# Performance work log

Measured on AMD Instinct MI355X. Metric: run time of the kernel, lower is better.

## Reference

```python
import jax, jax.numpy as jnp
import numpy as np

SEQ_LEN = 4096
INPUT_DIM = 768
DIM = 512
NUM_HEADS = 8
HEAD_DIM = DIM // NUM_HEADS
WINDOW_SIZE = 7
DILATION = 8
HALF_WINDOW = WINDOW_SIZE // 2  # 3
BIDIRECTIONAL = True


def _dilated_mask(seq_len):
    # allowed neighbors of query i: j = i + k*DILATION for k in [-HALF_WINDOW, HALF_WINDOW]
    # (only k<=0 if not bidirectional), clipped to [0, seq_len)
    idx = jnp.arange(seq_len)
    d = idx[None, :] - idx[:, None]  # j - i
    allowed = (d % DILATION == 0) & (jnp.abs(d) <= DILATION * HALF_WINDOW)
    if not BIDIRECTIONAL:
        allowed = allowed & (d <= 0)
    return jnp.where(allowed, 0.0, -jnp.inf).astype(jnp.float32)  # [S, S]


def setup_inputs() -> dict:
    key = jax.random.key(0)
    ks = jax.random.split(key, 6)
    s = 0.02
    return {
        "x": jax.random.normal(ks[0], (SEQ_LEN, INPUT_DIM), dtype=jnp.float32),
        "W_in": jax.random.normal(ks[1], (INPUT_DIM, DIM), dtype=jnp.float32) * s,
        "b_in": jnp.zeros((DIM,), dtype=jnp.float32),
        "W_tse": jax.random.normal(ks[2], (DIM, 3 * DIM), dtype=jnp.float32) * s,
        "W_out": jax.random.normal(ks[3], (DIM, DIM), dtype=jnp.float32) * s,
        "b_out": jnp.zeros((DIM,), dtype=jnp.float32),
    }


def reference(x, W_in, b_in, W_tse, W_out, b_out):
    S = x.shape[0]
    scale = HEAD_DIM ** -0.5
    h = x @ W_in + b_in                                   # [S, DIM]
    tse = (h @ W_tse).reshape(S, 3, NUM_HEADS, HEAD_DIM)   # [S, 3, H, hd]
    q, k, v = tse[:, 0], tse[:, 1], tse[:, 2]              # each [S, H, hd]
    scores = jnp.einsum("shd,thd->hst", q, k) * scale      # [H, S, S]
    scores = scores + _dilated_mask(S)[None, :, :]
    attn = jax.nn.softmax(scores, axis=-1)                 # [H, S, S]
    out = jnp.einsum("hst,thd->shd", attn, v)              # [S, H, hd]
    out = out.reshape(S, DIM)
    return out @ W_out + b_out                              # [S, DIM]
```

## Files before the change

### kernel.cpp

```cpp
#include <hip/hip_runtime.h>
#include <hip/hip_bf16.h>

#define S_LEN 4096
#define IN_DIM 768
#define D_DIM 512
#define N_HEADS 8
#define H_DIM 64
#define TSE_DIM 1536

typedef __attribute__((ext_vector_type(8))) short frag8;
typedef __attribute__((ext_vector_type(4))) float f32x4;

__device__ __forceinline__ unsigned short f2bfbits(float f) {
    unsigned int u = __float_as_uint(f);
    unsigned int r = (u + 0x7FFFu + ((u >> 16) & 1u)) >> 16;
    return (unsigned short)r;
}
__device__ __forceinline__ float bf2f(unsigned short b) {
    return __uint_as_float(((unsigned int)b) << 16);
}

__device__ __forceinline__ void gload_lds16(const void* g, void* l) {
    __builtin_amdgcn_global_load_lds(
        (const __attribute__((address_space(1))) unsigned int*)g,
        (__attribute__((address_space(3))) unsigned int*)l,
        16, 0, 0);
}

__global__ __launch_bounds__(256) void prep_kernel(
        const float4* __restrict__ x4, ushort4* __restrict__ xb4,
        const float* __restrict__ W_in,  unsigned short* __restrict__ WinT,
        const float* __restrict__ W_tse, unsigned short* __restrict__ WtseT,
        const float* __restrict__ W_out, unsigned short* __restrict__ WoutT) {
    __shared__ float tile[32][33];
    int b = blockIdx.x;
    if (b < 3072) {
        int i = b * 256 + threadIdx.x;
        float4 v = x4[i];
        ushort4 o;
        o.x = f2bfbits(v.x); o.y = f2bfbits(v.y);
        o.z = f2bfbits(v.z); o.w = f2bfbits(v.w);
        xb4[i] = o;
        return;
    }
    const float* in; unsigned short* out; int K, N, t;
    if (b < 3456)      { t = b - 3072; in = W_in;  out = WinT;  K = IN_DIM; N = D_DIM;  }
    else if (b < 4224) { t = b - 3456; in = W_tse; out = WtseT; K = D_DIM;  N = TSE_DIM;}
    else               { t = b - 4224; in = W_out; out = WoutT; K = D_DIM;  N = D_DIM;  }
    int ktiles = K / 32;
    int kb = (t % ktiles) * 32, nb = (t / ktiles) * 32;
    int tx = threadIdx.x & 31, ty = threadIdx.x >> 5;
    #pragma unroll
    for (int r = ty; r < 32; r += 8)
        tile[r][tx] = in[(size_t)(kb + r) * N + nb + tx];
    __syncthreads();
    #pragma unroll
    for (int r = ty; r < 32; r += 8)
        out[(size_t)(nb + r) * K + kb + tx] = f2bfbits(tile[tx][r]);
}

template<bool OUT_BF16, bool BIAS>
__global__ __launch_bounds__(256) void gemm_nt(
        const unsigned short* __restrict__ A,
        const unsigned short* __restrict__ Bt,
        const float* __restrict__ bias,
        void* __restrict__ C,
        int M, int N, int K) {
    __shared__ __align__(16) unsigned short As[2][64 * 32];
    __shared__ __align__(16) unsigned short Bs[2][64 * 32];

    const int bm = blockIdx.x * 64;
    const int bn = blockIdx.y * 64;
    const int lane = threadIdx.x & 63;
    const int wave = threadIdx.x >> 6;
    const int wr = wave >> 1;
    const int wc = wave & 1;
    const int fr = lane & 15;
    const int fg = lane >> 4;

    const int srow = lane >> 2;
    const int scol = (lane & 3) * 8;

    const unsigned short* agp = A  + (size_t)(bm + wave * 16 + srow) * K + scol;
    const unsigned short* bgp = Bt + (size_t)(bn + wave * 16 + srow) * K + scol;
    unsigned short* alp0 = &As[0][wave * 512];
    unsigned short* blp0 = &Bs[0][wave * 512];
    unsigned short* alp1 = &As[1][wave * 512];
    unsigned short* blp1 = &Bs[1][wave * 512];

    f32x4 acc[2][2];
    #pragma unroll
    for (int mi = 0; mi < 2; ++mi)
        #pragma unroll
        for (int ni = 0; ni < 2; ++ni)
            acc[mi][ni] = (f32x4)(0.f);

    const int nt = K >> 5;

    gload_lds16(agp, alp0);
    gload_lds16(bgp, blp0);
    __syncthreads();

    int cur = 0;
    for (int kt = 0; kt + 1 < nt; ++kt) {
        const int ko = (kt + 1) << 5;
        gload_lds16(agp + ko, cur ? alp0 : alp1);
        gload_lds16(bgp + ko, cur ? blp0 : blp1);

        frag8 a[2], b[2];
        #pragma unroll
        for (int mi = 0; mi < 2; ++mi)
            a[mi] = *(const frag8*)&As[cur][(wr * 32 + mi * 16 + fr) * 32 + fg * 8];
        #pragma unroll
        for (int ni = 0; ni < 2; ++ni)
            b[ni] = *(const frag8*)&Bs[cur][(wc * 32 + ni * 16 + fr) * 32 + fg * 8];
        #pragma unroll
        for (int mi = 0; mi < 2; ++mi)
            #pragma unroll
            for (int ni = 0; ni < 2; ++ni)
                acc[mi][ni] = __builtin_amdgcn_mfma_f32_16x16x32_bf16(
                        a[mi], b[ni], acc[mi][ni], 0, 0, 0);

        __syncthreads();
        cur ^= 1;
    }

    {
        frag8 a[2], b[2];
        #pragma unroll
        for (int mi = 0; mi < 2; ++mi)
            a[mi] = *(const frag8*)&As[cur][(wr * 32 + mi * 16 + fr) * 32 + fg * 8];
        #pragma unroll
        for (int ni = 0; ni < 2; ++ni)
            b[ni] = *(const frag8*)&Bs[cur][(wc * 32 + ni * 16 + fr) * 32 + fg * 8];
        #pragma unroll
        for (int mi = 0; mi < 2; ++mi)
            #pragma unroll
            for (int ni = 0; ni < 2; ++ni)
                acc[mi][ni] = __builtin_amdgcn_mfma_f32_16x16x32_bf16(
                        a[mi], b[ni], acc[mi][ni], 0, 0, 0);
    }

    #pragma unroll
    for (int mi = 0; mi < 2; ++mi) {
        int grow = bm + wr * 32 + mi * 16 + fg * 4;
        #pragma unroll
        for (int ni = 0; ni < 2; ++ni) {
            int gcol = bn + wc * 32 + ni * 16 + fr;
            float bv = BIAS ? bias[gcol] : 0.f;
            #pragma unroll
            for (int r = 0; r < 4; ++r) {
                float v = acc[mi][ni][r] + bv;
                if (OUT_BF16)
                    ((unsigned short*)C)[(size_t)(grow + r) * N + gcol] = f2bfbits(v);
                else
                    ((float*)C)[(size_t)(grow + r) * N + gcol] = v;
            }
        }
    }
}

__global__ __launch_bounds__(256) void attn_kernel(
        const unsigned short* __restrict__ tse, unsigned short* __restrict__ out) {
    const int s    = blockIdx.x * 4 + (threadIdx.x >> 6);
    const int lane = threadIdx.x & 63;
    const int off  = (lane >> 3) * H_DIM + (lane & 7) * 8;

    float qf[8];
    {
        frag8 q = *(const frag8*)(tse + (size_t)s * TSE_DIM + off);
        #pragma unroll
        for (int i = 0; i < 8; ++i) qf[i] = bf2f((unsigned short)q[i]);
    }

    float sc[7];
    #pragma unroll
    for (int j = 0; j < 7; ++j) {
        int t = s + (j - 3) * 8;
        bool valid = (t >= 0) && (t < S_LEN);
        float p = 0.f;
        if (valid) {
            frag8 k = *(const frag8*)(tse + (size_t)t * TSE_DIM + D_DIM + off);
            #pragma unroll
            for (int i = 0; i < 8; ++i) p += qf[i] * bf2f((unsigned short)k[i]);
        }
        p += __shfl_xor(p, 1, 64);
        p += __shfl_xor(p, 2, 64);
        p += __shfl_xor(p, 4, 64);
        sc[j] = valid ? p * 0.125f : -__builtin_inff();
    }

    float m = sc[0];
    #pragma unroll
    for (int j = 1; j < 7; ++j) m = fmaxf(m, sc[j]);

    float w[7], denom = 0.f;
    #pragma unroll
    for (int j = 0; j < 7; ++j) {
        w[j] = (sc[j] == -__builtin_inff()) ? 0.f : __expf(sc[j] - m);
        denom += w[j];
    }
    const float inv = 1.f / denom;

    float of[8];
    #pragma unroll
    for (int i = 0; i < 8; ++i) of[i] = 0.f;
    #pragma unroll
    for (int j = 0; j < 7; ++j) {
        int t = s + (j - 3) * 8;
        if (t >= 0 && t < S_LEN) {
            frag8 v = *(const frag8*)(tse + (size_t)t * TSE_DIM + 2 * D_DIM + off);
            #pragma unroll
            for (int i = 0; i < 8; ++i) of[i] += w[j] * bf2f((unsigned short)v[i]);
        }
    }

    frag8 o;
    #pragma unroll
    for (int i = 0; i < 8; ++i) o[i] = (short)f2bfbits(of[i] * inv);
    *(frag8*)(out + (size_t)s * D_DIM + off) = o;
}

extern "C" void kernel_launch(void* const* d_in, const int* in_sizes, int n_in,
                              void* d_out, int out_size, void* d_ws, size_t ws_size,
                              hipStream_t stream) {
    (void)in_sizes; (void)n_in; (void)out_size;
    const float* x     = (const float*)d_in[0];
    const float* W_in  = (const float*)d_in[1];
    const float* b_in  = (const float*)d_in[2];
    const float* W_tse = (const float*)d_in[3];
    const float* W_out = (const float*)d_in[4];
    const float* b_out = (const float*)d_in[5];

    char* p = (char*)d_ws;
    unsigned short* xb    = (unsigned short*)p; p += (size_t)S_LEN * IN_DIM * 2;
    unsigned short* WinT  = (unsigned short*)p; p += (size_t)D_DIM * IN_DIM * 2;
    unsigned short* WtseT = (unsigned short*)p; p += (size_t)TSE_DIM * D_DIM * 2;
    unsigned short* WoutT = (unsigned short*)p; p += (size_t)D_DIM * D_DIM * 2;
    unsigned short* h     = (unsigned short*)p; p += (size_t)S_LEN * D_DIM * 2;
    unsigned short* tse   = (unsigned short*)p; p += (size_t)S_LEN * TSE_DIM * 2;
    unsigned short* attn  = (unsigned short*)p; p += (size_t)S_LEN * D_DIM * 2;
    if ((size_t)(p - (char*)d_ws) > ws_size) return;

    prep_kernel<<<4480, 256, 0, stream>>>(
            (const float4*)x, (ushort4*)xb, W_in, WinT, W_tse, WtseT, W_out, WoutT);

    gemm_nt<true, true><<<dim3(S_LEN / 64, D_DIM / 64), 256, 0, stream>>>(
            xb, WinT, b_in, h, S_LEN, D_DIM, IN_DIM);
    gemm_nt<true, false><<<dim3(S_LEN / 64, TSE_DIM / 64), 256, 0, stream>>>(
            h, WtseT, nullptr, tse, S_LEN, TSE_DIM, D_DIM);
    attn_kernel<<<S_LEN / 4, 256, 0, stream>>>(tse, attn);
    gemm_nt<false, true><<<dim3(S_LEN / 64, D_DIM / 64), 256, 0, stream>>>(
            attn, WoutT, b_out, (float*)d_out, S_LEN, D_DIM, D_DIM);
}
```

Measured before the change: 53.03 us.

## Triple-buffer GEMM LDS tiles with manual vmcnt waits and single barrier

```diff
diff --git a/kernel.cpp b/kernel.cpp
--- a/kernel.cpp
+++ b/kernel.cpp
@@ -66,8 +66,8 @@
         const float* __restrict__ bias,
         void* __restrict__ C,
         int M, int N, int K) {
-    __shared__ __align__(16) unsigned short As[2][64 * 32];
-    __shared__ __align__(16) unsigned short Bs[2][64 * 32];
+    __shared__ __align__(16) unsigned short As[3][64 * 32];
+    __shared__ __align__(16) unsigned short Bs[3][64 * 32];
 
     const int bm = blockIdx.x * 64;
     const int bn = blockIdx.y * 64;
@@ -83,10 +83,8 @@
 
     const unsigned short* agp = A  + (size_t)(bm + wave * 16 + srow) * K + scol;
     const unsigned short* bgp = Bt + (size_t)(bn + wave * 16 + srow) * K + scol;
-    unsigned short* alp0 = &As[0][wave * 512];
-    unsigned short* blp0 = &Bs[0][wave * 512];
-    unsigned short* alp1 = &As[1][wave * 512];
-    unsigned short* blp1 = &Bs[1][wave * 512];
+    unsigned short* const alp = &As[0][wave * 512];
+    unsigned short* const blp = &Bs[0][wave * 512];
 
     f32x4 acc[2][2];
     #pragma unroll
@@ -97,42 +95,31 @@
 
     const int nt = K >> 5;
 
-    gload_lds16(agp, alp0);
-    gload_lds16(bgp, blp0);
-    __syncthreads();
-
-    int cur = 0;
-    for (int kt = 0; kt + 1 < nt; ++kt) {
-        const int ko = (kt + 1) << 5;
-        gload_lds16(agp + ko, cur ? alp0 : alp1);
-        gload_lds16(bgp + ko, cur ? blp0 : blp1);
-
+    gload_lds16(agp, alp);
+    gload_lds16(bgp, blp);
+    gload_lds16(agp + 32, alp + 2048);
+    gload_lds16(bgp + 32, blp + 2048);
+
+    for (int kt = 0; kt < nt; ++kt) {
+        if (kt == nt - 1) asm volatile("s_waitcnt vmcnt(0)" ::: "memory");
+        else              asm volatile("s_waitcnt vmcnt(2)" ::: "memory");
+        __builtin_amdgcn_s_barrier();
+        __builtin_amdgcn_sched_barrier(0);
+
+        if (kt + 2 < nt) {
+            const int sb = (kt + 2) % 3;
+            gload_lds16(agp + (size_t)(kt + 2) * 32, alp + sb * 2048);
+            gload_lds16(bgp + (size_t)(kt + 2) * 32, blp + sb * 2048);
+        }
+
+        const int cb = kt % 3;
         frag8 a[2], b[2];
         #pragma unroll
         for (int mi = 0; mi < 2; ++mi)
-            a[mi] = *(const frag8*)&As[cur][(wr * 32 + mi * 16 + fr) * 32 + fg * 8];
+            a[mi] = *(const frag8*)&As[cb][(wr * 32 + mi * 16 + fr) * 32 + fg * 8];
         #pragma unroll
         for (int ni = 0; ni < 2; ++ni)
-            b[ni] = *(const frag8*)&Bs[cur][(wc * 32 + ni * 16 + fr) * 32 + fg * 8];
-        #pragma unroll
-        for (int mi = 0; mi < 2; ++mi)
-            #pragma unroll
-            for (int ni = 0; ni < 2; ++ni)
-                acc[mi][ni] = __builtin_amdgcn_mfma_f32_16x16x32_bf16(
-                        a[mi], b[ni], acc[mi][ni], 0, 0, 0);
-
-        __syncthreads();
-        cur ^= 1;
-    }
-
-    {
-        frag8 a[2], b[2];
-        #pragma unroll
-        for (int mi = 0; mi < 2; ++mi)
-            a[mi] = *(const frag8*)&As[cur][(wr * 32 + mi * 16 + fr) * 32 + fg * 8];
-        #pragma unroll
-        for (int ni = 0; ni < 2; ++ni)
-            b[ni] = *(const frag8*)&Bs[cur][(wc * 32 + ni * 16 + fr) * 32 + fg * 8];
+            b[ni] = *(const frag8*)&Bs[cb][(wc * 32 + ni * 16 + fr) * 32 + fg * 8];
         #pragma unroll
         for (int mi = 0; mi < 2; ++mi)
             #pragma unroll
```

After: 56.01 us. 1.06x slower.

## Fold input projection into QKV weights via precombined W_in·W_tse GEMM

Applied to the files above, without the earlier changes.

```diff
diff --git a/kernel.cpp b/kernel.cpp
--- a/kernel.cpp
+++ b/kernel.cpp
@@ -29,34 +29,46 @@
 
 __global__ __launch_bounds__(256) void prep_kernel(
         const float4* __restrict__ x4, ushort4* __restrict__ xb4,
-        const float* __restrict__ W_in,  unsigned short* __restrict__ WinT,
+        const float4* __restrict__ Win4, ushort4* __restrict__ Winb4,
         const float* __restrict__ W_tse, unsigned short* __restrict__ WtseT,
-        const float* __restrict__ W_out, unsigned short* __restrict__ WoutT) {
+        const float* __restrict__ W_out, unsigned short* __restrict__ WoutT,
+        const float* __restrict__ b_in,  float* __restrict__ bias_tse) {
     __shared__ float tile[32][33];
     int b = blockIdx.x;
-    if (b < 3072) {
-        int i = b * 256 + threadIdx.x;
-        float4 v = x4[i];
+    if (b < 3456) {
+        const float4* src; ushort4* dst; int i;
+        if (b < 3072) { src = x4;   dst = xb4;   i = b * 256 + threadIdx.x; }
+        else          { src = Win4; dst = Winb4; i = (b - 3072) * 256 + threadIdx.x; }
+        float4 v = src[i];
         ushort4 o;
         o.x = f2bfbits(v.x); o.y = f2bfbits(v.y);
         o.z = f2bfbits(v.z); o.w = f2bfbits(v.w);
-        xb4[i] = o;
+        dst[i] = o;
         return;
     }
-    const float* in; unsigned short* out; int K, N, t;
-    if (b < 3456)      { t = b - 3072; in = W_in;  out = WinT;  K = IN_DIM; N = D_DIM;  }
-    else if (b < 4224) { t = b - 3456; in = W_tse; out = WtseT; K = D_DIM;  N = TSE_DIM;}
-    else               { t = b - 4224; in = W_out; out = WoutT; K = D_DIM;  N = D_DIM;  }
-    int ktiles = K / 32;
-    int kb = (t % ktiles) * 32, nb = (t / ktiles) * 32;
-    int tx = threadIdx.x & 31, ty = threadIdx.x >> 5;
-    #pragma unroll
-    for (int r = ty; r < 32; r += 8)
-        tile[r][tx] = in[(size_t)(kb + r) * N + nb + tx];
-    __syncthreads();
-    #pragma unroll
-    for (int r = ty; r < 32; r += 8)
-        out[(size_t)(nb + r) * K + kb + tx] = f2bfbits(tile[tx][r]);
+    if (b < 4480) {
+        const float* in; unsigned short* out; int K, N, t;
+        if (b < 4224) { t = b - 3456; in = W_tse; out = WtseT; K = D_DIM; N = TSE_DIM; }
+        else          { t = b - 4224; in = W_out; out = WoutT; K = D_DIM; N = D_DIM;  }
+        int ktiles = K / 32;
+        int kb = (t % ktiles) * 32, nb = (t / ktiles) * 32;
+        int tx = threadIdx.x & 31, ty = threadIdx.x >> 5;
+        #pragma unroll
+        for (int r = ty; r < 32; r += 8)
+            tile[r][tx] = in[(size_t)(kb + r) * N + nb + tx];
+        __syncthreads();
+        #pragma unroll
+        for (int r = ty; r < 32; r += 8)
+            out[(size_t)(nb + r) * K + kb + tx] = f2bfbits(tile[tx][r]);
+        return;
+    }
+    {
+        int j = (b - 4480) * 256 + threadIdx.x;
+        float acc = 0.f;
+        for (int k = 0; k < D_DIM; ++k)
+            acc += b_in[k] * W_tse[(size_t)k * TSE_DIM + j];
+        bias_tse[j] = acc;
+    }
 }
 
 template<bool OUT_BF16, bool BIAS>
@@ -233,22 +245,25 @@
     const float* b_out = (const float*)d_in[5];
 
     char* p = (char*)d_ws;
-    unsigned short* xb    = (unsigned short*)p; p += (size_t)S_LEN * IN_DIM * 2;
-    unsigned short* WinT  = (unsigned short*)p; p += (size_t)D_DIM * IN_DIM * 2;
-    unsigned short* WtseT = (unsigned short*)p; p += (size_t)TSE_DIM * D_DIM * 2;
-    unsigned short* WoutT = (unsigned short*)p; p += (size_t)D_DIM * D_DIM * 2;
-    unsigned short* h     = (unsigned short*)p; p += (size_t)S_LEN * D_DIM * 2;
-    unsigned short* tse   = (unsigned short*)p; p += (size_t)S_LEN * TSE_DIM * 2;
-    unsigned short* attn  = (unsigned short*)p; p += (size_t)S_LEN * D_DIM * 2;
+    unsigned short* xb     = (unsigned short*)p; p += (size_t)S_LEN * IN_DIM * 2;
+    unsigned short* Winb   = (unsigned short*)p; p += (size_t)IN_DIM * D_DIM * 2;
+    unsigned short* WtseT  = (unsigned short*)p; p += (size_t)TSE_DIM * D_DIM * 2;
+    unsigned short* WoutT  = (unsigned short*)p; p += (size_t)D_DIM * D_DIM * 2;
+    unsigned short* WcombT = (unsigned short*)p; p += (size_t)TSE_DIM * IN_DIM * 2;
+    float*          biasT  = (float*)p;          p += (size_t)TSE_DIM * 4;
+    unsigned short* tse    = (unsigned short*)p; p += (size_t)S_LEN * TSE_DIM * 2;
+    unsigned short* attn   = (unsigned short*)p; p += (size_t)S_LEN * D_DIM * 2;
     if ((size_t)(p - (char*)d_ws) > ws_size) return;
 
-    prep_kernel<<<4480, 256, 0, stream>>>(
-            (const float4*)x, (ushort4*)xb, W_in, WinT, W_tse, WtseT, W_out, WoutT);
-
-    gemm_nt<true, true><<<dim3(S_LEN / 64, D_DIM / 64), 256, 0, stream>>>(
-            xb, WinT, b_in, h, S_LEN, D_DIM, IN_DIM);
-    gemm_nt<true, false><<<dim3(S_LEN / 64, TSE_DIM / 64), 256, 0, stream>>>(
-            h, WtseT, nullptr, tse, S_LEN, TSE_DIM, D_DIM);
+    prep_kernel<<<4486, 256, 0, stream>>>(
+            (const float4*)x, (ushort4*)xb,
+            (const float4*)W_in, (ushort4*)Winb,
+            W_tse, WtseT, W_out, WoutT, b_in, biasT);
+
+    gemm_nt<true, false><<<dim3(TSE_DIM / 64, IN_DIM / 64), 256, 0, stream>>>(
+            WtseT, Winb, nullptr, WcombT, TSE_DIM, IN_DIM, D_DIM);
+    gemm_nt<true, true><<<dim3(S_LEN / 64, TSE_DIM / 64), 256, 0, stream>>>(
+            xb, WcombT, biasT, tse, S_LEN, TSE_DIM, IN_DIM);
     attn_kernel<<<S_LEN / 4, 256, 0, stream>>>(tse, attn);
     gemm_nt<false, true><<<dim3(S_LEN / 64, D_DIM / 64), 256, 0, stream>>>(
             attn, WoutT, b_out, (float*)d_out, S_LEN, D_DIM, D_DIM);
```

Result: slower. 95.60 us (+80.3%).

## Fuse dilated attention into output projection GEMM via LDS-resident attention tile

Applied to the files above, without the earlier changes.

```diff
diff --git a/kernel.cpp b/kernel.cpp
--- a/kernel.cpp
+++ b/kernel.cpp
@@ -160,65 +160,142 @@
     }
 }
 
-__global__ __launch_bounds__(256) void attn_kernel(
-        const unsigned short* __restrict__ tse, unsigned short* __restrict__ out) {
-    const int s    = blockIdx.x * 4 + (threadIdx.x >> 6);
+__global__ __launch_bounds__(256) void gemm3_attn(
+        const unsigned short* __restrict__ tse,
+        const unsigned short* __restrict__ Bt,
+        const float* __restrict__ bias,
+        float* __restrict__ C) {
+    __shared__ __align__(16) unsigned short Ab[64 * 512];
+    __shared__ __align__(16) unsigned short Bs[2][64 * 32];
+
+    const int bm = blockIdx.x * 64;
+    const int bn = blockIdx.y * 64;
     const int lane = threadIdx.x & 63;
-    const int off  = (lane >> 3) * H_DIM + (lane & 7) * 8;
-
-    float qf[8];
-    {
-        frag8 q = *(const frag8*)(tse + (size_t)s * TSE_DIM + off);
-        #pragma unroll
-        for (int i = 0; i < 8; ++i) qf[i] = bf2f((unsigned short)q[i]);
-    }
-
-    float sc[7];
-    #pragma unroll
-    for (int j = 0; j < 7; ++j) {
-        int t = s + (j - 3) * 8;
-        bool valid = (t >= 0) && (t < S_LEN);
-        float p = 0.f;
-        if (valid) {
-            frag8 k = *(const frag8*)(tse + (size_t)t * TSE_DIM + D_DIM + off);
-            #pragma unroll
-            for (int i = 0; i < 8; ++i) p += qf[i] * bf2f((unsigned short)k[i]);
-        }
-        p += __shfl_xor(p, 1, 64);
-        p += __shfl_xor(p, 2, 64);
-        p += __shfl_xor(p, 4, 64);
-        sc[j] = valid ? p * 0.125f : -__builtin_inff();
-    }
-
-    float m = sc[0];
-    #pragma unroll
-    for (int j = 1; j < 7; ++j) m = fmaxf(m, sc[j]);
-
-    float w[7], denom = 0.f;
-    #pragma unroll
-    for (int j = 0; j < 7; ++j) {
-        w[j] = (sc[j] == -__builtin_inff()) ? 0.f : __expf(sc[j] - m);
-        denom += w[j];
-    }
-    const float inv = 1.f / denom;
-
-    float of[8];
-    #pragma unroll
-    for (int i = 0; i < 8; ++i) of[i] = 0.f;
-    #pragma unroll
-    for (int j = 0; j < 7; ++j) {
-        int t = s + (j - 3) * 8;
-        if (t >= 0 && t < S_LEN) {
-            frag8 v = *(const frag8*)(tse + (size_t)t * TSE_DIM + 2 * D_DIM + off);
-            #pragma unroll
-            for (int i = 0; i < 8; ++i) of[i] += w[j] * bf2f((unsigned short)v[i]);
-        }
-    }
-
-    frag8 o;
-    #pragma unroll
-    for (int i = 0; i < 8; ++i) o[i] = (short)f2bfbits(of[i] * inv);
-    *(frag8*)(out + (size_t)s * D_DIM + off) = o;
+    const int wave = threadIdx.x >> 6;
+    const int wr = wave >> 1;
+    const int wc = wave & 1;
+    const int fr = lane & 15;
+    const int fg = lane >> 4;
+    const int srow = lane >> 2;
+    const int scol = (lane & 3) * 8;
+
+    const int off = (lane >> 3) * H_DIM + (lane & 7) * 8;
+    for (int ir = 0; ir < 16; ++ir) {
+        const int s = bm + wave * 16 + ir;
+
+        float qf[8];
+        {
+            frag8 q = *(const frag8*)(tse + (size_t)s * TSE_DIM + off);
+            #pragma unroll
+            for (int i = 0; i < 8; ++i) qf[i] = bf2f((unsigned short)q[i]);
+        }
+
+        float sc[7];
+        #pragma unroll
+        for (int j = 0; j < 7; ++j) {
+            int t = s + (j - 3) * 8;
+            bool valid = (t >= 0) && (t < S_LEN);
+            float p = 0.f;
+            if (valid) {
+                frag8 k = *(const frag8*)(tse + (size_t)t * TSE_DIM + D_DIM + off);
+                #pragma unroll
+                for (int i = 0; i < 8; ++i) p += qf[i] * bf2f((unsigned short)k[i]);
+            }
+            p += __shfl_xor(p, 1, 64);
+            p += __shfl_xor(p, 2, 64);
+            p += __shfl_xor(p, 4, 64);
+            sc[j] = valid ? p * 0.125f : -__builtin_inff();
+        }
+
+        float m = sc[0];
+        #pragma unroll
+        for (int j = 1; j < 7; ++j) m = fmaxf(m, sc[j]);
+
+        float w[7], denom = 0.f;
+        #pragma unroll
+        for (int j = 0; j < 7; ++j) {
+            w[j] = (sc[j] == -__builtin_inff()) ? 0.f : __expf(sc[j] - m);
+            denom += w[j];
+        }
+        const float inv = 1.f / denom;
+
+        float of[8];
+        #pragma unroll
+        for (int i = 0; i < 8; ++i) of[i] = 0.f;
+        #pragma unroll
+        for (int j = 0; j < 7; ++j) {
+            int t = s + (j - 3) * 8;
+            if (t >= 0 && t < S_LEN) {
+                frag8 v = *(const frag8*)(tse + (size_t)t * TSE_DIM + 2 * D_DIM + off);
+                #pragma unroll
+                for (int i = 0; i < 8; ++i) of[i] += w[j] * bf2f((unsigned short)v[i]);
+            }
+        }
+
+        frag8 o;
+        #pragma unroll
+        for (int i = 0; i < 8; ++i) o[i] = (short)f2bfbits(of[i] * inv);
+
+        const int lrow = wave * 16 + ir;
+        *(frag8*)((char*)Ab + (size_t)lrow * 1024 + ((off * 2) ^ ((lrow & 7) << 4))) = o;
+    }
+
+    const unsigned short* bgp = Bt + (size_t)(bn + wave * 16 + srow) * D_DIM + scol;
+    unsigned short* blp0 = &Bs[0][wave * 512];
+    unsigned short* blp1 = &Bs[1][wave * 512];
+
+    gload_lds16(bgp, blp0);
+    __syncthreads();
+
+    f32x4 acc[2][2];
+    #pragma unroll
+    for (int mi = 0; mi < 2; ++mi)
+        #pragma unroll
+        for (int ni = 0; ni < 2; ++ni)
+            acc[mi][ni] = (f32x4)(0.f);
+
+    const int nt = D_DIM >> 5;
+    const char* abase = (const char*)Ab;
+    int cur = 0;
+    for (int kt = 0; kt < nt; ++kt) {
+        if (kt + 1 < nt)
+            gload_lds16(bgp + ((kt + 1) << 5), cur ? blp0 : blp1);
+
+        frag8 a[2], b[2];
+        #pragma unroll
+        for (int mi = 0; mi < 2; ++mi) {
+            const int row = wr * 32 + mi * 16 + fr;
+            a[mi] = *(const frag8*)(abase + (size_t)row * 1024 +
+                                    ((kt * 64 + fg * 16) ^ ((fr & 7) << 4)));
+        }
+        #pragma unroll
+        for (int ni = 0; ni < 2; ++ni)
+            b[ni] = *(const frag8*)&Bs[cur][(wc * 32 + ni * 16 + fr) * 32 + fg * 8];
+        #pragma unroll
+        for (int mi = 0; mi < 2; ++mi)
+            #pragma unroll
+            for (int ni = 0; ni < 2; ++ni)
+                acc[mi][ni] = __builtin_amdgcn_mfma_f32_16x16x32_bf16(
+                        a[mi], b[ni], acc[mi][ni], 0, 0, 0);
+
+        if (kt + 1 < nt) {
+            __syncthreads();
+            cur ^= 1;
+        }
+    }
+
+    #pragma unroll
+    for (int mi = 0; mi < 2; ++mi) {
+        int grow = bm + wr * 32 + mi * 16 + fg * 4;
+        #pragma unroll
+        for (int ni = 0; ni < 2; ++ni) {
+            int gcol = bn + wc * 32 + ni * 16 + fr;
+            float bv = bias[gcol];
+            #pragma unroll
+            for (int r = 0; r < 4; ++r)
+                C[(size_t)(grow + r) * D_DIM + gcol] = acc[mi][ni][r] + bv;
+        }
+    }
 }
 
 extern "C" void kernel_launch(void* const* d_in, const int* in_sizes, int n_in,
@@ -239,7 +316,6 @@
     unsigned short* WoutT = (unsigned short*)p; p += (size_t)D_DIM * D_DIM * 2;
     unsigned short* h     = (unsigned short*)p; p += (size_t)S_LEN * D_DIM * 2;
     unsigned short* tse   = (unsigned short*)p; p += (size_t)S_LEN * TSE_DIM * 2;
-    unsigned short* attn  = (unsigned short*)p; p += (size_t)S_LEN * D_DIM * 2;
     if ((size_t)(p - (char*)d_ws) > ws_size) return;
 
     prep_kernel<<<4480, 256, 0, stream>>>(
@@ -249,7 +325,6 @@
             xb, WinT, b_in, h, S_LEN, D_DIM, IN_DIM);
     gemm_nt<true, false><<<dim3(S_LEN / 64, TSE_DIM / 64), 256, 0, stream>>>(
             h, WtseT, nullptr, tse, S_LEN, TSE_DIM, D_DIM);
-    attn_kernel<<<S_LEN / 4, 256, 0, stream>>>(tse, attn);
-    gemm_nt<false, true><<<dim3(S_LEN / 64, D_DIM / 64), 256, 0, stream>>>(
-            attn, WoutT, b_out, (float*)d_out, S_LEN, D_DIM, D_DIM);
-}
+    gemm3_attn<<<dim3(S_LEN / 64, D_DIM / 64), 256, 0, stream>>>(
+            tse, WoutT, b_out, (float*)d_out);
+}
```

Measured after the change: 106.8 us. +101.4%, slower.
